# Performance work log

Measured on AMD Instinct MI355X. Metric: run time of the kernel, lower is better.

## Reference

```python
import jax, jax.numpy as jnp
import numpy as np

B, C, BAND, K, NUM_OUT, HID = 1024, 62, 5, 2, 16, 10


def _gate(x, w, b):
    # Basic: relu(softmax(conv(x), dim=1) * x); conv kernel covers full CxC map -> [B, band]
    s = jnp.einsum('bihw,oihw->bo', x, w) + b
    g = jax.nn.softmax(s, axis=1)
    return jax.nn.relu(g[:, :, None, None] * x)


def _spd(x):
    # signal2spd applied per band slice (E2R patch length 1 since epochs==band_num)
    # x: [B, band, c, c] -> per-band trace-normalized covariance SPD
    c = x.shape[-1]
    xc = x - x.mean(-1, keepdims=True)
    cov = jnp.einsum('bkij,bkil->bkjl', xc, xc) / (c - 1)
    tra = jnp.trace(cov, axis1=-2, axis2=-1)[..., None, None]
    return cov / tra + 1e-5 * jnp.eye(c, dtype=x.dtype)


def _branch(x, cw, cb, lw, lb):
    # Sequential(depthwise 1x1 conv, Linear(c,c) on last dim, Sigmoid)
    y = x * cw[None, :, None, None] + cb[None, :, None, None]
    y = jnp.einsum('bkic,oc->bkio', y, lw) + lb
    return jax.nn.sigmoid(y)


def _attn(z, w1, b1, w2):
    # Attentionadj: softmax over band axis of a 2-layer scorer, weighted sum -> [B,c,c]
    h = jnp.tanh(jnp.einsum('bkic,hc->bkih', z, w1) + b1)
    w = jnp.einsum('bkih,oh->bkio', h, w2)  # [B, band, c, 1]
    beta = jax.nn.softmax(w, axis=1)
    return (beta * z).sum(1)


def _cheb_gcn(x, L, gc_w, gc_b):
    # Chebynet K=2 with supports T0=I, T1=L; GraphConvolution: adj @ x @ W + b
    out = x @ gc_w[0] + gc_b[0]
    out = out + jnp.einsum('bij,bjf->bif', L, x @ gc_w[1]) + gc_b[1]
    return jax.nn.relu(out)


def setup_inputs():
    key = jax.random.key(0)
    ks = jax.random.split(key, 24)
    f = lambda i, shape, s=0.05: (s * jax.random.normal(ks[i], shape, dtype=jnp.float32))
    return {
        'de': jax.random.normal(ks[0], (B, C, BAND), dtype=jnp.float32),
        'pcc': jax.random.normal(ks[1], (B, C, C, BAND), dtype=jnp.float32),
        'A': jax.random.normal(ks[2], (B, BAND, C, C), dtype=jnp.float32),
        'conv_w': f(3, (BAND, BAND, C, C)),
        'conv_b': f(4, (BAND,)),
        'hconv_w': f(5, (BAND,), 1.0),
        'hconv_b': f(6, (BAND,)),
        'hlin_w': f(7, (C, C)),
        'hlin_b': f(8, (C,)),
        'econv_w': f(9, (BAND,), 1.0),
        'econv_b': f(10, (BAND,)),
        'elin_w': f(11, (C, C)),
        'elin_b': f(12, (C,)),
        'att_w1': f(13, (HID, C), 0.3),
        'att_b1': f(14, (HID,)),
        'att_w2': f(15, (1, HID), 0.3),
        'gc_w': f(16, (K, BAND, NUM_OUT), 0.3),
        'gc_b': f(17, (K, NUM_OUT)),
        'wpar': jnp.ones((1,), dtype=jnp.float32),
        'fc_w': f(18, (C, C * NUM_OUT)),
        'fc_b': f(19, (C,)),
        'bn_g': jnp.ones((C,), dtype=jnp.float32),
        'bn_b': jnp.zeros((C,), dtype=jnp.float32),
        'fc4_w': f(20, (2, C), 0.3),
        'fc4_b': f(21, (2,)),
    }


def reference(de, pcc, A, conv_w, conv_b, hconv_w, hconv_b, hlin_w, hlin_b,
              econv_w, econv_b, elin_w, elin_b, att_w1, att_b1, att_w2,
              gc_w, gc_b, wpar, fc_w, fc_b, bn_g, bn_b, fc4_w, fc4_b):
    # Basic: gated functional / structural adjacencies
    fadj = _gate(jnp.transpose(pcc, (0, 3, 1, 2)), conv_w, conv_b)  # [B,band,c,c]
    sadj = _gate(A, conv_w, conv_b)
    # E2R covariance SPD per band, then average
    com = (_spd(fadj) + _spd(sadj)) / 2  # [B,band,c,c]
    # hidden / essential sigmoid-gated branches + attention pooling over bands
    hidden = _attn(_branch(com, hconv_w, hconv_b, hlin_w, hlin_b), att_w1, att_b1, att_w2)
    essential = _attn(_branch(com, econv_w, econv_b, elin_w, elin_b), att_w1, att_b1, att_w2)
    # Chebyshev GCN over de features with each learned adjacency
    h = _cheb_gcn(de, hidden, gc_w, gc_b)
    e = _cheb_gcn(de, essential, gc_w, gc_b)
    wnorm = jnp.exp(wpar[0]) / jnp.sum(jnp.exp(wpar))
    feature = jax.nn.relu((h + e) / 2 * wnorm)  # [B, C, NUM_OUT]
    flat = feature.reshape(feature.shape[0], -1)
    # fc62: Linear + BatchNorm1d (training-mode batch stats) + Dropout(eval=id) + Sigmoid
    z = flat @ fc_w.T + fc_b
    z = (z - z.mean(0)) / jnp.sqrt(z.var(0) + 1e-5) * bn_g + bn_b
    output1 = jax.nn.sigmoid(z)
    output = output1 @ fc4_w.T + fc4_b
    return (output1, output)
```

## Files before the change

### kernel.cpp

```cpp
#include <hip/hip_runtime.h>
#include <math.h>

#define NB    1024
#define NC    62
#define NBAND 5
#define NOUT  16
#define NHID  10
#define ZSTR  72
#define CLS   72
#define CSLOT (64 * CLS)
#define XTW   34

typedef __attribute__((ext_vector_type(4))) float f32x4;
typedef __attribute__((ext_vector_type(8))) _Float16 f16x8;
typedef __attribute__((ext_vector_type(2))) __fp16 fp16v2;

__device__ __forceinline__ unsigned int pk2u(float x, float y) {
  const fp16v2 v = __builtin_amdgcn_cvt_pkrtz(x, y);
  return __builtin_bit_cast(unsigned int, v);
}

__global__ __launch_bounds__(256, 2) void k_fused(
    const float* __restrict__ pcc, const float* __restrict__ Aadj,
    const float* __restrict__ hlin_w, const float* __restrict__ elin_w,
    const float* __restrict__ hconv_w, const float* __restrict__ hconv_b,
    const float* __restrict__ hlin_b,
    const float* __restrict__ econv_w, const float* __restrict__ econv_b,
    const float* __restrict__ elin_b,
    const float* __restrict__ att_w1, const float* __restrict__ att_b1,
    const float* __restrict__ att_w2,
    const float* __restrict__ de, const float* __restrict__ gc_w,
    const float* __restrict__ gc_b, const float* __restrict__ fc_w,
    const float* __restrict__ fc_b, float* __restrict__ zmat) {
  const int b = (blockIdx.x & 7) * 128 + (blockIdx.x >> 3);
  __shared__ __align__(16) _Float16 pHcom[NBAND * CSLOT];
  __shared__ __align__(16) unsigned int XcT[64 * XTW];
  __shared__ __align__(16) _Float16 zS[4][16 * ZSTR];
  __shared__ float deS[NC * NBAND + 2];
  __shared__ float rsumL[2][64], lbL[2][64];
  __shared__ float cwL[2][8], cbL[2][8];
  __shared__ float red4a[4], red4b[4];

  const int tid = threadIdx.x;
  const int wave = tid >> 6, lane = tid & 63;
  const int p = tid >> 3, q8 = tid & 7, c0 = q8 * 8;
  const bool act = (p < 31);
  const int r0 = 2 * p, r1 = r0 + 1;
  const int mrow = lane & 15, g = lane >> 4;

  if (tid < 128) {
    const int pbr = tid >> 6, col = tid & 63;
    const float* lwsrc = pbr ? elin_w : hlin_w;
    float s = 0.f;
    if (col < NC) {
      const float* rowp = lwsrc + col * NC;
#pragma unroll
      for (int e = 0; e < 31; ++e) {
        const float2 v = *reinterpret_cast<const float2*>(rowp + 2 * e);
        s += v.x + v.y;
      }
    }
    rsumL[pbr][col] = s;
    lbL[pbr][col] = (col < NC) ? (pbr ? elin_b : hlin_b)[col] : 0.f;
  }
  if (tid < NBAND) {
    cwL[0][tid] = hconv_w[tid]; cbL[0][tid] = hconv_b[tid];
    cwL[1][tid] = econv_w[tid]; cbL[1][tid] = econv_b[tid];
  }
  for (int t = tid; t < NC * NBAND; t += 256) deS[t] = de[(size_t)b * (NC * NBAND) + t];

  float ld0[8], ld1[8];
  float lA0[8], lA1[8];

  auto center = [&](float (&a0)[8], float (&a1)[8], float* red) -> void {
    float s0 = 0.f, s1 = 0.f;
#pragma unroll
    for (int u = 0; u < 8; ++u) { s0 += a0[u]; s1 += a1[u]; }
    s0 += __shfl_xor(s0, 1, 64); s0 += __shfl_xor(s0, 2, 64); s0 += __shfl_xor(s0, 4, 64);
    s1 += __shfl_xor(s1, 1, 64); s1 += __shfl_xor(s1, 2, 64); s1 += __shfl_xor(s1, 4, 64);
    const float m0 = s0 * (1.f / NC), m1 = s1 * (1.f / NC);
    float sq = 0.f;
#pragma unroll
    for (int u = 0; u < 8; ++u) {
      const bool in = act && (c0 + u < NC);
      const float cv0 = in ? (a0[u] - m0) : 0.f;
      const float cv1 = in ? (a1[u] - m1) : 0.f;
      a0[u] = cv0;
      a1[u] = cv1;
      sq += cv0 * cv0 + cv1 * cv1;
    }
#pragma unroll
    for (int off = 1; off < 64; off <<= 1) sq += __shfl_xor(sq, off, 64);
    if (lane == 0) red[wave] = sq;
  };

  auto xct_write = [&](const float (&a0)[8], const float (&a1)[8], float sc) -> void {
#pragma unroll
    for (int u = 0; u < 8; ++u)
      XcT[(c0 + u) * XTW + p] = pk2u(sc * a0[u], sc * a1[u]);
  };

  auto fragread = [&](int row, int s) -> f16x8 {
    const unsigned int* pp = &XcT[row * XTW + 16 * s + 4 * g];
    const uint2 a = *reinterpret_cast<const uint2*>(pp);
    const uint2 b2 = *reinterpret_cast<const uint2*>(pp + 2);
    const uint4 v = make_uint4(a.x, a.y, b2.x, b2.y);
    return __builtin_bit_cast(f16x8, v);
  };

  {
    const float4* src = reinterpret_cast<const float4*>(pcc + (size_t)b * (NC * NC * NBAND));
#pragma unroll
    for (int it = 0; it < 19; ++it) {
      const int fidx = tid + it * 256;
      if (fidx < 4805) {
        const float4 v = src[fidx];
        const int g0 = 4 * fidx;
        int i = g0 / 310;
        int rem = g0 - i * 310;
        int j = rem / 5;
        int k = rem - j * 5;
        const float vals[4] = {v.x, v.y, v.z, v.w};
#pragma unroll
        for (int e = 0; e < 4; ++e) {
          pHcom[k * CSLOT + i * CLS + j] = (_Float16)fmaxf(vals[e], 0.f);
          if (++k == 5) { k = 0; if (++j == NC) { j = 0; ++i; } }
        }
      }
    }
  }
  __syncthreads();

#pragma unroll 1
  for (int kb = 0; kb < NBAND; ++kb) {
    const int bk = b * NBAND + kb;

#pragma unroll
    for (int u = 0; u < 8; ++u) { lA0[u] = 0.f; lA1[u] = 0.f; }
    if (act) {
      const float* a0p = Aadj + ((size_t)bk * NC + r0) * NC + c0;
      const float* a1p = Aadj + ((size_t)bk * NC + r1) * NC + c0;
#pragma unroll
      for (int e = 0; e < 4; ++e) {
        const int c = c0 + 2 * e;
        if (c + 1 < NC) {
          const float2 v0 = *reinterpret_cast<const float2*>(a0p + 2 * e);
          const float2 v1 = *reinterpret_cast<const float2*>(a1p + 2 * e);
          lA0[2 * e] = v0.x; lA0[2 * e + 1] = v0.y;
          lA1[2 * e] = v1.x; lA1[2 * e + 1] = v1.y;
        } else if (c < NC) {
          lA0[2 * e] = a0p[2 * e];
          lA1[2 * e] = a1p[2 * e];
        }
      }
    }

#pragma unroll
    for (int u = 0; u < 8; ++u) { ld0[u] = 0.f; ld1[u] = 0.f; }
    if (act) {
      const _Float16* ph = pHcom + kb * CSLOT;
#pragma unroll
      for (int u = 0; u < 8; ++u) {
        const int c = c0 + u;
        if (c < NC) {
          ld0[u] = (float)ph[r0 * CLS + c];
          ld1[u] = (float)ph[r1 * CLS + c];
        }
      }
    }
    center(ld0, ld1, red4a);
    __syncthreads();

    const float tra0 = red4a[0] + red4a[1] + red4a[2] + red4a[3];
    xct_write(ld0, ld1, sqrtf(0.5f / tra0));
    __syncthreads();

    f32x4 acc[4];
#pragma unroll
    for (int n = 0; n < 4; ++n) acc[n] = (f32x4){0.f, 0.f, 0.f, 0.f};
    {
      const f16x8 A0 = fragread(16 * wave + mrow, 0);
      const f16x8 A1 = fragread(16 * wave + mrow, 1);
#pragma unroll
      for (int n = 0; n < 4; ++n) {
        const f16x8 B0 = fragread(16 * n + mrow, 0);
        const f16x8 B1 = fragread(16 * n + mrow, 1);
        acc[n] = __builtin_amdgcn_mfma_f32_16x16x32_f16(A0, B0, acc[n], 0, 0, 0);
        acc[n] = __builtin_amdgcn_mfma_f32_16x16x32_f16(A1, B1, acc[n], 0, 0, 0);
      }
    }

#pragma unroll
    for (int u = 0; u < 8; ++u) { lA0[u] = fmaxf(lA0[u], 0.f); lA1[u] = fmaxf(lA1[u], 0.f); }
    center(lA0, lA1, red4b);
    __syncthreads();

    const float tra1 = red4b[0] + red4b[1] + red4b[2] + red4b[3];
    xct_write(lA0, lA1, sqrtf(0.5f / tra1));
    __syncthreads();

    {
      const f16x8 A0 = fragread(16 * wave + mrow, 0);
      const f16x8 A1 = fragread(16 * wave + mrow, 1);
#pragma unroll
      for (int n = 0; n < 4; ++n) {
        const f16x8 B0 = fragread(16 * n + mrow, 0);
        const f16x8 B1 = fragread(16 * n + mrow, 1);
        acc[n] = __builtin_amdgcn_mfma_f32_16x16x32_f16(A0, B0, acc[n], 0, 0, 0);
        acc[n] = __builtin_amdgcn_mfma_f32_16x16x32_f16(A1, B1, acc[n], 0, 0, 0);
      }
    }

    {
      _Float16* comL = pHcom + kb * CSLOT;
#pragma unroll
      for (int reg = 0; reg < 4; ++reg) {
        const int r = 16 * wave + 4 * g + reg;
#pragma unroll
        for (int n = 0; n < 4; ++n) {
          float v = acc[n][reg];
          if (n == wave && mrow == 4 * g + reg) v += 1e-5f;
          comL[r * CLS + 16 * n + mrow] = (_Float16)v;
        }
      }
    }
  }

  f16x8 W1f[2];
#pragma unroll
  for (int s = 0; s < 2; ++s) {
    unsigned int pk[4] = {0u, 0u, 0u, 0u};
    if (mrow < NHID) {
#pragma unroll
      for (int e = 0; e < 4; ++e) {
        const int c = 32 * s + 8 * g + 2 * e;
        if (c + 1 < NC) {
          const float2 v = *reinterpret_cast<const float2*>(att_w1 + mrow * NC + c);
          pk[e] = pk2u(v.x, v.y);
        }
      }
    }
    W1f[s] = __builtin_bit_cast(f16x8, make_uint4(pk[0], pk[1], pk[2], pk[3]));
  }
  const float b1R = (mrow < NHID) ? att_b1[mrow] : 0.f;
  const float w2R = (mrow < NHID) ? att_w2[mrow] : 0.f;

  f16x8 T1f[2];
  float t0R[4], gb1R2;
  {
    float gw1c[5], gw0c[5];
#pragma unroll
    for (int q = 0; q < 5; ++q) {
      gw0c[q] = gc_w[q * NOUT + mrow];
      gw1c[q] = gc_w[(NBAND + q) * NOUT + mrow];
    }
    const float gb0 = gc_b[mrow];
    gb1R2 = gc_b[NOUT + mrow];
#pragma unroll
    for (int s = 0; s < 2; ++s) {
      unsigned int pk[4];
#pragma unroll
      for (int e2 = 0; e2 < 4; ++e2) {
        const int j0 = 32 * s + 8 * g + 2 * e2, j1 = j0 + 1;
        float a = 0.f, bb = 0.f;
        if (j0 < NC) {
#pragma unroll
          for (int q = 0; q < 5; ++q) a += deS[j0 * 5 + q] * gw1c[q];
        }
        if (j1 < NC) {
#pragma unroll
          for (int q = 0; q < 5; ++q) bb += deS[j1 * 5 + q] * gw1c[q];
        }
        pk[e2] = pk2u(a, bb);
      }
      T1f[s] = __builtin_bit_cast(f16x8, make_uint4(pk[0], pk[1], pk[2], pk[3]));
    }
#pragma unroll
    for (int reg = 0; reg < 4; ++reg) {
      const int r = 16 * wave + 4 * g + reg;
      float t = 0.f;
      if (r < NC) {
        t = gb0;
#pragma unroll
        for (int q = 0; q < 5; ++q) t += deS[r * 5 + q] * gw0c[q];
      }
      t0R[reg] = t;
    }
  }

  _Float16* zSw = &zS[wave][0];
  auto z_frag = [&](int s) -> f16x8 {
    return __builtin_bit_cast(f16x8,
        *reinterpret_cast<const uint4*>(zSw + mrow * ZSTR + 32 * s + 8 * g));
  };
  auto a_frag = [&](int kb, int s) -> f16x8 {
    return __builtin_bit_cast(f16x8,
        *reinterpret_cast<const uint4*>(pHcom + kb * CSLOT + (16 * wave + mrow) * CLS + 32 * s + 8 * g));
  };

  float facc[4] = {0.f, 0.f, 0.f, 0.f};

#pragma unroll 1
  for (int br = 0; br < 2; ++br) {
    const float* __restrict__ lwsrc = br ? elin_w : hlin_w;

    f16x8 Bf[2][4];
    float rsumR[4], lbR[4];
#pragma unroll
    for (int n = 0; n < 4; ++n) {
      const int col = 16 * n + mrow;
      rsumR[n] = rsumL[br][col];
      lbR[n] = lbL[br][col];
#pragma unroll
      for (int s = 0; s < 2; ++s) {
        unsigned int pk[4] = {0u, 0u, 0u, 0u};
        if (col < NC) {
#pragma unroll
          for (int e = 0; e < 4; ++e) {
            const int c = 32 * s + 8 * g + 2 * e;
            if (c + 1 < NC) {
              const float2 v = *reinterpret_cast<const float2*>(lwsrc + col * NC + c);
              pk[e] = pk2u(v.x, v.y);
            }
          }
        }
        Bf[s][n] = __builtin_bit_cast(f16x8, make_uint4(pk[0], pk[1], pk[2], pk[3]));
      }
    }

    f32x4 oacc[4];
#pragma unroll
    for (int n = 0; n < 4; ++n) oacc[n] = (f32x4){0.f, 0.f, 0.f, 0.f};
    float denom[4] = {0.f, 0.f, 0.f, 0.f};
    float mrun[4] = {-1e30f, -1e30f, -1e30f, -1e30f};

#pragma unroll 1
    for (int kb = 0; kb < NBAND; ++kb) {
      const f16x8 A0 = a_frag(kb, 0);
      const f16x8 A1 = a_frag(kb, 1);
      f32x4 acc[4];
#pragma unroll
      for (int n = 0; n < 4; ++n) {
        acc[n] = __builtin_amdgcn_mfma_f32_16x16x32_f16(A0, Bf[0][n], (f32x4){0.f, 0.f, 0.f, 0.f}, 0, 0, 0);
        acc[n] = __builtin_amdgcn_mfma_f32_16x16x32_f16(A1, Bf[1][n], acc[n], 0, 0, 0);
      }

      const float ck = cwL[br][kb], dk = cbL[br][kb];
#pragma unroll
      for (int n = 0; n < 4; ++n) {
        const float base = dk * rsumR[n] + lbR[n];
#pragma unroll
        for (int reg = 0; reg < 4; ++reg) {
          const float zv = 1.f / (1.f + __expf(-(ck * acc[n][reg] + base)));
          acc[n][reg] = zv;
          zSw[(4 * g + reg) * ZSTR + 16 * n + mrow] = (_Float16)zv;
        }
      }

      float scr[4];
      {
        const f16x8 Z0 = z_frag(0);
        const f16x8 Z1 = z_frag(1);
        f32x4 pacc = __builtin_amdgcn_mfma_f32_16x16x32_f16(Z0, W1f[0], (f32x4){0.f, 0.f, 0.f, 0.f}, 0, 0, 0);
        pacc = __builtin_amdgcn_mfma_f32_16x16x32_f16(Z1, W1f[1], pacc, 0, 0, 0);
#pragma unroll
        for (int reg = 0; reg < 4; ++reg) {
          const float ex = __expf(2.f * (pacc[reg] + b1R));
          float v = w2R * (1.f - 2.f / (ex + 1.f));
          v += __shfl_xor(v, 1, 64);
          v += __shfl_xor(v, 2, 64);
          v += __shfl_xor(v, 4, 64);
          v += __shfl_xor(v, 8, 64);
          scr[reg] = v;
        }
      }

#pragma unroll
      for (int reg = 0; reg < 4; ++reg) {
        const float sc = scr[reg];
        const float nm = fmaxf(mrun[reg], sc);
        const float f = __expf(mrun[reg] - nm), e = __expf(sc - nm);
        denom[reg] = denom[reg] * f + e;
#pragma unroll
        for (int n = 0; n < 4; ++n)
          oacc[n][reg] = oacc[n][reg] * f + e * acc[n][reg];
        mrun[reg] = nm;
      }
    }

#pragma unroll
    for (int reg = 0; reg < 4; ++reg) {
      const float inv = 1.f / denom[reg];
#pragma unroll
      for (int n = 0; n < 4; ++n)
        zSw[(4 * g + reg) * ZSTR + 16 * n + mrow] = (_Float16)(oacc[n][reg] * inv);
    }

    {
      const f16x8 H0 = z_frag(0);
      const f16x8 H1 = z_frag(1);
      f32x4 ch = __builtin_amdgcn_mfma_f32_16x16x32_f16(H0, T1f[0], (f32x4){0.f, 0.f, 0.f, 0.f}, 0, 0, 0);
      ch = __builtin_amdgcn_mfma_f32_16x16x32_f16(H1, T1f[1], ch, 0, 0, 0);
#pragma unroll
      for (int reg = 0; reg < 4; ++reg)
        facc[reg] += 0.5f * fmaxf(t0R[reg] + ch[reg] + gb1R2, 0.f);
    }
  }

  __syncthreads();
  float* featS = reinterpret_cast<float*>(XcT);
  float* red2  = reinterpret_cast<float*>(XcT) + 1024;
#pragma unroll
  for (int reg = 0; reg < 4; ++reg) {
    const int r = 16 * wave + 4 * g + reg;
    featS[r * NOUT + mrow] = facc[reg];
  }
  __syncthreads();
  {
    const int n = tid >> 2, qq = tid & 3;
    float ps = 0.f;
    if (n < NC) {
      const float* fw = fc_w + n * (NC * NOUT) + qq * 248;
      const float* fs = featS + qq * 248;
      for (int m = 0; m < 248; ++m) ps += fs[m] * fw[m];
    }
    red2[tid] = ps;
    __syncthreads();
    if (tid < NC) {
      zmat[(size_t)b * NC + tid] =
          red2[tid * 4] + red2[tid * 4 + 1] + red2[tid * 4 + 2] + red2[tid * 4 + 3] + fc_b[tid];
    }
  }
}

__global__ __launch_bounds__(256) void k_bnstats(
    const float* __restrict__ zmat, const float* __restrict__ bn_g,
    const float* __restrict__ bn_b, float* __restrict__ bnp) {
  const int n = blockIdx.x;
  __shared__ float rs[256], rq[256];
  const int tid = threadIdx.x;
  float s = 0.f, sq = 0.f;
  for (int r = tid; r < NB; r += 256) {
    const float v = zmat[r * NC + n];
    s += v;
    sq += v * v;
  }
  rs[tid] = s; rq[tid] = sq;
  __syncthreads();
  for (int st = 128; st > 0; st >>= 1) {
    if (tid < st) { rs[tid] += rs[tid + st]; rq[tid] += rq[tid + st]; }
    __syncthreads();
  }
  if (tid == 0) {
    const float mean = rs[0] * (1.f / NB);
    const float var = rq[0] * (1.f / NB) - mean * mean;
    const float sc = bn_g[n] * rsqrtf(var + 1e-5f);
    bnp[2 * n] = sc;
    bnp[2 * n + 1] = bn_b[n] - mean * sc;
  }
}

__global__ __launch_bounds__(64) void k_bn_out(
    const float* __restrict__ zmat, const float* __restrict__ bnp,
    const float* __restrict__ fc4_w, const float* __restrict__ fc4_b,
    float* __restrict__ out) {
  const int b = blockIdx.x;
  const int lane = threadIdx.x;
  float o1 = 0.f;
  if (lane < NC) {
    float z = zmat[b * NC + lane];
    z = z * bnp[2 * lane] + bnp[2 * lane + 1];
    o1 = 1.f / (1.f + __expf(-z));
    out[b * NC + lane] = o1;
  }
  float p0 = (lane < NC) ? o1 * fc4_w[lane] : 0.f;
  float p1 = (lane < NC) ? o1 * fc4_w[NC + lane] : 0.f;
#pragma unroll
  for (int off = 32; off > 0; off >>= 1) {
    p0 += __shfl_down(p0, off, 64);
    p1 += __shfl_down(p1, off, 64);
  }
  if (lane == 0) {
    out[NB * NC + b * 2 + 0] = p0 + fc4_b[0];
    out[NB * NC + b * 2 + 1] = p1 + fc4_b[1];
  }
}

extern "C" void kernel_launch(void* const* d_in, const int* in_sizes, int n_in,
                              void* d_out, int out_size, void* d_ws, size_t ws_size,
                              hipStream_t stream) {
  const float* de      = (const float*)d_in[0];
  const float* pcc     = (const float*)d_in[1];
  const float* Aadj    = (const float*)d_in[2];
  const float* hconv_w = (const float*)d_in[5];
  const float* hconv_b = (const float*)d_in[6];
  const float* hlin_w  = (const float*)d_in[7];
  const float* hlin_b  = (const float*)d_in[8];
  const float* econv_w = (const float*)d_in[9];
  const float* econv_b = (const float*)d_in[10];
  const float* elin_w  = (const float*)d_in[11];
  const float* elin_b  = (const float*)d_in[12];
  const float* att_w1  = (const float*)d_in[13];
  const float* att_b1  = (const float*)d_in[14];
  const float* att_w2  = (const float*)d_in[15];
  const float* gc_w    = (const float*)d_in[16];
  const float* gc_b    = (const float*)d_in[17];
  const float* fc_w    = (const float*)d_in[19];
  const float* fc_b    = (const float*)d_in[20];
  const float* bn_g    = (const float*)d_in[21];
  const float* bn_b    = (const float*)d_in[22];
  const float* fc4_w   = (const float*)d_in[23];
  const float* fc4_b   = (const float*)d_in[24];

  float* ws   = (float*)d_ws;
  float* zmat = ws;
  float* bnp  = zmat + (size_t)NB * NC;

  k_fused<<<NB, 256, 0, stream>>>(pcc, Aadj, hlin_w, elin_w,
      hconv_w, hconv_b, hlin_b,
      econv_w, econv_b, elin_b,
      att_w1, att_b1, att_w2,
      de, gc_w, gc_b, fc_w, fc_b, zmat);
  k_bnstats<<<NC, 256, 0, stream>>>(zmat, bn_g, bn_b, bnp);
  k_bn_out<<<NB, 64, 0, stream>>>(zmat, bnp, fc4_w, fc4_b, (float*)d_out);
}
```

Baseline: 116.6 us.

## Double-buffer covariance tiles, prepack fp16 weights in init kernel, vectorize fc dot

The two per-band covariance passes now write to separate XcT buffers, and the trace normalization moves from the write stage to the final combine. This removes two block-wide barriers per band and lets the second centering overlap the first MFMA pass. A new single-block init kernel prepacks the linear and attention weights into fp16 and computes the row sums once, so every block loads ready-made fragments with uint4 reads instead of converting them itself. The final fc dot product uses float4 loads. The costs are extra LDS for the second buffer, an extra kernel launch, and unscaled fp16 values in XcT, which risks losing precision or overflowing.

```diff
diff --git a/kernel.cpp b/kernel.cpp
--- a/kernel.cpp
+++ b/kernel.cpp
@@ -20,24 +20,59 @@
   return __builtin_bit_cast(unsigned int, v);
 }
 
+__global__ __launch_bounds__(256) void k_init(
+    const float* __restrict__ hlin_w, const float* __restrict__ elin_w,
+    const float* __restrict__ att_w1,
+    unsigned int* __restrict__ lwHg, unsigned int* __restrict__ w1Hg,
+    float* __restrict__ rsumG) {
+  const int tid = threadIdx.x;
+  for (int t = tid; t < 2 * 64 * 32; t += 256) {
+    const int brx = t >> 11, rem = t & 2047, o = rem >> 5, cp = rem & 31;
+    const float* lwsrc = brx ? elin_w : hlin_w;
+    float lo = 0.f, hi = 0.f;
+    if (o < NC) {
+      const int c = 2 * cp;
+      if (c < NC)     lo = lwsrc[o * NC + c];
+      if (c + 1 < NC) hi = lwsrc[o * NC + c + 1];
+    }
+    lwHg[t] = pk2u(lo, hi);
+  }
+  for (int t = tid; t < 16 * 32; t += 256) {
+    const int h = t >> 5, op = t & 31;
+    float lo = 0.f, hi = 0.f;
+    if (h < NHID) {
+      if (2 * op < NC)     lo = att_w1[h * NC + 2 * op];
+      if (2 * op + 1 < NC) hi = att_w1[h * NC + 2 * op + 1];
+    }
+    w1Hg[t] = pk2u(lo, hi);
+  }
+  if (tid < 128) {
+    const int pbr = tid >> 6, col = tid & 63;
+    const float* lwsrc = pbr ? elin_w : hlin_w;
+    float s = 0.f;
+    if (col < NC)
+      for (int c = 0; c < NC; ++c) s += lwsrc[col * NC + c];
+    rsumG[pbr * 64 + col] = s;
+  }
+}
+
 __global__ __launch_bounds__(256, 2) void k_fused(
     const float* __restrict__ pcc, const float* __restrict__ Aadj,
-    const float* __restrict__ hlin_w, const float* __restrict__ elin_w,
+    const unsigned int* __restrict__ lwHg, const unsigned int* __restrict__ w1Hg,
+    const float* __restrict__ rsumG,
     const float* __restrict__ hconv_w, const float* __restrict__ hconv_b,
     const float* __restrict__ hlin_b,
     const float* __restrict__ econv_w, const float* __restrict__ econv_b,
     const float* __restrict__ elin_b,
-    const float* __restrict__ att_w1, const float* __restrict__ att_b1,
-    const float* __restrict__ att_w2,
+    const float* __restrict__ att_b1, const float* __restrict__ att_w2,
     const float* __restrict__ de, const float* __restrict__ gc_w,
     const float* __restrict__ gc_b, const float* __restrict__ fc_w,
     const float* __restrict__ fc_b, float* __restrict__ zmat) {
   const int b = (blockIdx.x & 7) * 128 + (blockIdx.x >> 3);
   __shared__ __align__(16) _Float16 pHcom[NBAND * CSLOT];
-  __shared__ __align__(16) unsigned int XcT[64 * XTW];
+  __shared__ __align__(16) unsigned int XcT[2][64 * XTW];
   __shared__ __align__(16) _Float16 zS[4][16 * ZSTR];
   __shared__ float deS[NC * NBAND + 2];
-  __shared__ float rsumL[2][64], lbL[2][64];
   __shared__ float cwL[2][8], cbL[2][8];
   __shared__ float red4a[4], red4b[4];
 
@@ -48,21 +83,6 @@
   const int r0 = 2 * p, r1 = r0 + 1;
   const int mrow = lane & 15, g = lane >> 4;
 
-  if (tid < 128) {
-    const int pbr = tid >> 6, col = tid & 63;
-    const float* lwsrc = pbr ? elin_w : hlin_w;
-    float s = 0.f;
-    if (col < NC) {
-      const float* rowp = lwsrc + col * NC;
-#pragma unroll
-      for (int e = 0; e < 31; ++e) {
-        const float2 v = *reinterpret_cast<const float2*>(rowp + 2 * e);
-        s += v.x + v.y;
-      }
-    }
-    rsumL[pbr][col] = s;
-    lbL[pbr][col] = (col < NC) ? (pbr ? elin_b : hlin_b)[col] : 0.f;
-  }
   if (tid < NBAND) {
     cwL[0][tid] = hconv_w[tid]; cbL[0][tid] = hconv_b[tid];
     cwL[1][tid] = econv_w[tid]; cbL[1][tid] = econv_b[tid];
@@ -94,18 +114,30 @@
     if (lane == 0) red[wave] = sq;
   };
 
-  auto xct_write = [&](const float (&a0)[8], const float (&a1)[8], float sc) -> void {
+  auto xct_write = [&](unsigned int* X, const float (&a0)[8], const float (&a1)[8]) -> void {
 #pragma unroll
     for (int u = 0; u < 8; ++u)
-      XcT[(c0 + u) * XTW + p] = pk2u(sc * a0[u], sc * a1[u]);
+      X[(c0 + u) * XTW + p] = pk2u(a0[u], a1[u]);
   };
 
-  auto fragread = [&](int row, int s) -> f16x8 {
-    const unsigned int* pp = &XcT[row * XTW + 16 * s + 4 * g];
+  auto fragread = [&](const unsigned int* X, int row, int s) -> f16x8 {
+    const unsigned int* pp = &X[row * XTW + 16 * s + 4 * g];
     const uint2 a = *reinterpret_cast<const uint2*>(pp);
     const uint2 b2 = *reinterpret_cast<const uint2*>(pp + 2);
     const uint4 v = make_uint4(a.x, a.y, b2.x, b2.y);
     return __builtin_bit_cast(f16x8, v);
+  };
+
+  auto syrk = [&](const unsigned int* X, f32x4 (&acc)[4]) -> void {
+    const f16x8 A0 = fragread(X, 16 * wave + mrow, 0);
+    const f16x8 A1 = fragread(X, 16 * wave + mrow, 1);
+#pragma unroll
+    for (int n = 0; n < 4; ++n) {
+      const f16x8 B0 = fragread(X, 16 * n + mrow, 0);
+      const f16x8 B1 = fragread(X, 16 * n + mrow, 1);
+      acc[n] = __builtin_amdgcn_mfma_f32_16x16x32_f16(A0, B0, acc[n], 0, 0, 0);
+      acc[n] = __builtin_amdgcn_mfma_f32_16x16x32_f16(A1, B1, acc[n], 0, 0, 0);
+    }
   };
 
   {
@@ -169,56 +201,36 @@
       }
     }
     center(ld0, ld1, red4a);
+    xct_write(XcT[0], ld0, ld1);
     __syncthreads();
 
     const float tra0 = red4a[0] + red4a[1] + red4a[2] + red4a[3];
-    xct_write(ld0, ld1, sqrtf(0.5f / tra0));
-    __syncthreads();
-
-    f32x4 acc[4];
-#pragma unroll
-    for (int n = 0; n < 4; ++n) acc[n] = (f32x4){0.f, 0.f, 0.f, 0.f};
-    {
-      const f16x8 A0 = fragread(16 * wave + mrow, 0);
-      const f16x8 A1 = fragread(16 * wave + mrow, 1);
-#pragma unroll
-      for (int n = 0; n < 4; ++n) {
-        const f16x8 B0 = fragread(16 * n + mrow, 0);
-        const f16x8 B1 = fragread(16 * n + mrow, 1);
-        acc[n] = __builtin_amdgcn_mfma_f32_16x16x32_f16(A0, B0, acc[n], 0, 0, 0);
-        acc[n] = __builtin_amdgcn_mfma_f32_16x16x32_f16(A1, B1, acc[n], 0, 0, 0);
-      }
-    }
+    f32x4 acc0[4];
+#pragma unroll
+    for (int n = 0; n < 4; ++n) acc0[n] = (f32x4){0.f, 0.f, 0.f, 0.f};
+    syrk(XcT[0], acc0);
 
 #pragma unroll
     for (int u = 0; u < 8; ++u) { lA0[u] = fmaxf(lA0[u], 0.f); lA1[u] = fmaxf(lA1[u], 0.f); }
     center(lA0, lA1, red4b);
+    xct_write(XcT[1], lA0, lA1);
     __syncthreads();
 
     const float tra1 = red4b[0] + red4b[1] + red4b[2] + red4b[3];
-    xct_write(lA0, lA1, sqrtf(0.5f / tra1));
-    __syncthreads();
+    f32x4 acc1[4];
+#pragma unroll
+    for (int n = 0; n < 4; ++n) acc1[n] = (f32x4){0.f, 0.f, 0.f, 0.f};
+    syrk(XcT[1], acc1);
 
     {
-      const f16x8 A0 = fragread(16 * wave + mrow, 0);
-      const f16x8 A1 = fragread(16 * wave + mrow, 1);
-#pragma unroll
-      for (int n = 0; n < 4; ++n) {
-        const f16x8 B0 = fragread(16 * n + mrow, 0);
-        const f16x8 B1 = fragread(16 * n + mrow, 1);
-        acc[n] = __builtin_amdgcn_mfma_f32_16x16x32_f16(A0, B0, acc[n], 0, 0, 0);
-        acc[n] = __builtin_amdgcn_mfma_f32_16x16x32_f16(A1, B1, acc[n], 0, 0, 0);
-      }
-    }
-
-    {
+      const float s0 = 0.5f / tra0, s1 = 0.5f / tra1;
       _Float16* comL = pHcom + kb * CSLOT;
 #pragma unroll
       for (int reg = 0; reg < 4; ++reg) {
         const int r = 16 * wave + 4 * g + reg;
 #pragma unroll
         for (int n = 0; n < 4; ++n) {
-          float v = acc[n][reg];
+          float v = acc0[n][reg] * s0 + acc1[n][reg] * s1;
           if (n == wave && mrow == 4 * g + reg) v += 1e-5f;
           comL[r * CLS + 16 * n + mrow] = (_Float16)v;
         }
@@ -229,18 +241,8 @@
   f16x8 W1f[2];
 #pragma unroll
   for (int s = 0; s < 2; ++s) {
-    unsigned int pk[4] = {0u, 0u, 0u, 0u};
-    if (mrow < NHID) {
-#pragma unroll
-      for (int e = 0; e < 4; ++e) {
-        const int c = 32 * s + 8 * g + 2 * e;
-        if (c + 1 < NC) {
-          const float2 v = *reinterpret_cast<const float2*>(att_w1 + mrow * NC + c);
-          pk[e] = pk2u(v.x, v.y);
-        }
-      }
-    }
-    W1f[s] = __builtin_bit_cast(f16x8, make_uint4(pk[0], pk[1], pk[2], pk[3]));
+    const uint4 v = *reinterpret_cast<const uint4*>(w1Hg + mrow * 32 + s * 16 + g * 4);
+    W1f[s] = __builtin_bit_cast(f16x8, v);
   }
   const float b1R = (mrow < NHID) ? att_b1[mrow] : 0.f;
   const float w2R = (mrow < NHID) ? att_w2[mrow] : 0.f;
@@ -302,29 +304,19 @@
 
 #pragma unroll 1
   for (int br = 0; br < 2; ++br) {
-    const float* __restrict__ lwsrc = br ? elin_w : hlin_w;
+    const float* __restrict__ lb = br ? elin_b : hlin_b;
 
     f16x8 Bf[2][4];
     float rsumR[4], lbR[4];
 #pragma unroll
     for (int n = 0; n < 4; ++n) {
       const int col = 16 * n + mrow;
-      rsumR[n] = rsumL[br][col];
-      lbR[n] = lbL[br][col];
+      rsumR[n] = rsumG[br * 64 + col];
+      lbR[n] = (col < NC) ? lb[col] : 0.f;
 #pragma unroll
       for (int s = 0; s < 2; ++s) {
-        unsigned int pk[4] = {0u, 0u, 0u, 0u};
-        if (col < NC) {
-#pragma unroll
-          for (int e = 0; e < 4; ++e) {
-            const int c = 32 * s + 8 * g + 2 * e;
-            if (c + 1 < NC) {
-              const float2 v = *reinterpret_cast<const float2*>(lwsrc + col * NC + c);
-              pk[e] = pk2u(v.x, v.y);
-            }
-          }
-        }
-        Bf[s][n] = __builtin_bit_cast(f16x8, make_uint4(pk[0], pk[1], pk[2], pk[3]));
+        const uint4 v = *reinterpret_cast<const uint4*>(lwHg + br * 2048 + col * 32 + s * 16 + g * 4);
+        Bf[s][n] = __builtin_bit_cast(f16x8, v);
       }
     }
 
@@ -420,9 +412,13 @@
     const int n = tid >> 2, qq = tid & 3;
     float ps = 0.f;
     if (n < NC) {
-      const float* fw = fc_w + n * (NC * NOUT) + qq * 248;
-      const float* fs = featS + qq * 248;
-      for (int m = 0; m < 248; ++m) ps += fs[m] * fw[m];
+      const float4* fw4 = reinterpret_cast<const float4*>(fc_w + n * (NC * NOUT));
+      const float4* fs4 = reinterpret_cast<const float4*>(featS);
+      for (int mm = 0; mm < 62; ++mm) {
+        const float4 a = fs4[mm * 4 + qq];
+        const float4 w = fw4[mm * 4 + qq];
+        ps += a.x * w.x + a.y * w.y + a.z * w.z + a.w * w.w;
+      }
     }
     red2[tid] = ps;
     __syncthreads();
@@ -515,11 +511,15 @@
   float* ws   = (float*)d_ws;
   float* zmat = ws;
   float* bnp  = zmat + (size_t)NB * NC;
-
-  k_fused<<<NB, 256, 0, stream>>>(pcc, Aadj, hlin_w, elin_w,
+  unsigned int* lwHg = (unsigned int*)(bnp + 128);
+  unsigned int* w1Hg = lwHg + 4096;
+  float* rsumG = (float*)(w1Hg + 512);
+
+  k_init<<<1, 256, 0, stream>>>(hlin_w, elin_w, att_w1, lwHg, w1Hg, rsumG);
+  k_fused<<<NB, 256, 0, stream>>>(pcc, Aadj, lwHg, w1Hg, rsumG,
       hconv_w, hconv_b, hlin_b,
       econv_w, econv_b, elin_b,
-      att_w1, att_b1, att_w2,
+      att_b1, att_w2,
       de, gc_w, gc_b, fc_w, fc_b, zmat);
   k_bnstats<<<NC, 256, 0, stream>>>(zmat, bn_g, bn_b, bnp);
   k_bn_out<<<NB, 64, 0, stream>>>(zmat, bnp, fc4_w, fc4_b, (float*)d_out);
```

Result: faster. 110.2 us (-5.5%).
